# Performance work log

Measured on AMD Instinct MI355X. Metric: run time of the kernel, lower is better.

The kernel has to match this reference:

```python
import jax, jax.numpy as jnp
import numpy as np

N_NODES = 50000
N_EDGES = 800000
D_IN = 64
F1 = 64
F2 = 64
D_HID = 100


def setup_inputs() -> dict:
    key = jax.random.key(0)
    ks = jax.random.split(key, 12)
    x = jax.random.normal(ks[0], (N_NODES, D_IN), dtype=jnp.float32)
    edge_src = jax.random.randint(ks[1], (N_EDGES,), 0, N_NODES, dtype=jnp.int32)
    edge_dst = jax.random.randint(ks[2], (N_EDGES,), 0, N_NODES, dtype=jnp.int32)
    # stands in for pre-normalized GCN adjacency values (D^-1/2 (A+I) D^-1/2)
    edge_weight = jax.random.uniform(ks[3], (N_EDGES,), dtype=jnp.float32)
    def glorot(k, shape):
        lim = np.sqrt(6.0 / (shape[0] + shape[1]))
        return jax.random.uniform(k, shape, jnp.float32, -lim, lim)
    W1 = glorot(ks[4], (D_IN, F1))
    b1 = jnp.zeros((F1,), jnp.float32)
    W2 = glorot(ks[5], (F1, F2))
    b2 = jnp.zeros((F2,), jnp.float32)
    Wd = glorot(ks[6], (F2, D_HID))
    bd = jnp.zeros((D_HID,), jnp.float32)
    Wo = glorot(ks[7], (D_HID, 1))
    bo = jnp.zeros((1,), jnp.float32)
    return {"x": x, "edge_src": edge_src, "edge_dst": edge_dst,
            "edge_weight": edge_weight, "W1": W1, "b1": b1, "W2": W2,
            "b2": b2, "Wd": Wd, "bd": bd, "Wo": Wo, "bo": bo}


def _gcn_conv(x, edge_src, edge_dst, edge_weight, W, b):
    # spektral GCNConv: out = swish(A_norm @ (X @ W) + b)
    h = x @ W                                        # [N, F]
    msg = h[edge_src] * edge_weight[:, None]          # [E, F] gather + scale
    agg = jax.ops.segment_sum(msg, edge_dst, num_segments=N_NODES)  # [N, F]
    return jax.nn.swish(agg + b)


def reference(x, edge_src, edge_dst, edge_weight, W1, b1, W2, b2, Wd, bd, Wo, bo):
    h = _gcn_conv(x, edge_src, edge_dst, edge_weight, W1, b1)
    h = _gcn_conv(h, edge_src, edge_dst, edge_weight, W2, b2)
    h = jax.nn.swish(h @ Wd + bd)                    # Dense(100, swish)
    return jax.nn.sigmoid(h @ Wo + bo)               # Dense(1, sigmoid) -> [N, 1]
```

## Files before the change

### kernel.cpp

```cpp
#include <hip/hip_runtime.h>
#include <hip/hip_fp16.h>

#define N_NODES 50000
#define N_EDGES 800000
#define D 64
#define DHID 100
#define NTILES (N_NODES / 16)
#define NCT 7
#define CAP 32
#define SPILL_MAX 8192
#define NGROUPS 4
#define NSLICES 780
#define FILL_BLOCKS (NGROUPS * NSLICES)
#define MM_BLOCKS ((NTILES + 3) / 4)
#define DST_PER_GROUP (N_NODES / NGROUPS)
#define FSTRIDE (NSLICES * 256)
#define KMAX 5

typedef unsigned short ushort;
typedef unsigned int uint;
typedef __attribute__((ext_vector_type(8))) short s16x8;
typedef __attribute__((ext_vector_type(4))) float f32x4;

#define MFMA16(A, B, C) __builtin_amdgcn_mfma_f32_16x16x32_bf16((A), (B), (C), 0, 0, 0)

__device__ __forceinline__ float swishf(float x) { return x / (1.0f + __expf(-x)); }

__device__ __forceinline__ ushort f2bf(float f) {
    uint u = __float_as_uint(f);
    uint r = (u + 0x7fffu + ((u >> 16) & 1u)) >> 16;
    return (ushort)r;
}
__device__ __forceinline__ float bf2f(ushort h) { return __uint_as_float((uint)h << 16); }
__device__ __forceinline__ float bf_lo(uint d) { return __uint_as_float(d << 16); }
__device__ __forceinline__ float bf_hi(uint d) { return __uint_as_float(d & 0xffff0000u); }

__device__ __forceinline__ float hwf(uint e) {
    return __half2float(__ushort_as_half((ushort)(e >> 16)));
}

__device__ __forceinline__ void accum8(float* acc, uint4 v, float w) {
    acc[0] = fmaf(w, bf_lo(v.x), acc[0]);
    acc[1] = fmaf(w, bf_hi(v.x), acc[1]);
    acc[2] = fmaf(w, bf_lo(v.y), acc[2]);
    acc[3] = fmaf(w, bf_hi(v.y), acc[3]);
    acc[4] = fmaf(w, bf_lo(v.z), acc[4]);
    acc[5] = fmaf(w, bf_hi(v.z), acc[5]);
    acc[6] = fmaf(w, bf_lo(v.w), acc[6]);
    acc[7] = fmaf(w, bf_hi(v.w), acc[7]);
}

__device__ __forceinline__ void gather_body(const ushort* __restrict__ H,
                                            uint4 eA, uint4 eB, int degv,
                                            int j, int fg, float* acc) {
#pragma unroll
    for (int t = 0; t < 8; ++t) acc[t] = 0.f;
    const int sA = j * 4, sB = 16 + j * 4;
    bool pA = sA < degv, pB = sB < degv;
    uint4 vA0, vA1, vA2, vA3, vB0, vB1, vB2, vB3;
    float wA0 = 0, wA1 = 0, wA2 = 0, wA3 = 0;
    float wB0 = 0, wB1 = 0, wB2 = 0, wB3 = 0;
    if (pA) {
        wA0 = hwf(eA.x);
        wA1 = (sA + 1 < degv) ? hwf(eA.y) : 0.f;
        wA2 = (sA + 2 < degv) ? hwf(eA.z) : 0.f;
        wA3 = (sA + 3 < degv) ? hwf(eA.w) : 0.f;
        uint i0 = min(eA.x & 0xffffu, (uint)(N_NODES - 1));
        uint i1 = min(eA.y & 0xffffu, (uint)(N_NODES - 1));
        uint i2 = min(eA.z & 0xffffu, (uint)(N_NODES - 1));
        uint i3 = min(eA.w & 0xffffu, (uint)(N_NODES - 1));
        vA0 = *((const uint4*)(H + ((size_t)i0 << 6) + (fg << 3)));
        vA1 = *((const uint4*)(H + ((size_t)i1 << 6) + (fg << 3)));
        vA2 = *((const uint4*)(H + ((size_t)i2 << 6) + (fg << 3)));
        vA3 = *((const uint4*)(H + ((size_t)i3 << 6) + (fg << 3)));
    }
    if (pB) {
        wB0 = hwf(eB.x);
        wB1 = (sB + 1 < degv) ? hwf(eB.y) : 0.f;
        wB2 = (sB + 2 < degv) ? hwf(eB.z) : 0.f;
        wB3 = (sB + 3 < degv) ? hwf(eB.w) : 0.f;
        uint i0 = min(eB.x & 0xffffu, (uint)(N_NODES - 1));
        uint i1 = min(eB.y & 0xffffu, (uint)(N_NODES - 1));
        uint i2 = min(eB.z & 0xffffu, (uint)(N_NODES - 1));
        uint i3 = min(eB.w & 0xffffu, (uint)(N_NODES - 1));
        vB0 = *((const uint4*)(H + ((size_t)i0 << 6) + (fg << 3)));
        vB1 = *((const uint4*)(H + ((size_t)i1 << 6) + (fg << 3)));
        vB2 = *((const uint4*)(H + ((size_t)i2 << 6) + (fg << 3)));
        vB3 = *((const uint4*)(H + ((size_t)i3 << 6) + (fg << 3)));
    }
    if (pA) {
        accum8(acc, vA0, wA0);
        accum8(acc, vA1, wA1);
        accum8(acc, vA2, wA2);
        accum8(acc, vA3, wA3);
    }
    if (pB) {
        accum8(acc, vB0, wB0);
        accum8(acc, vB1, wB1);
        accum8(acc, vB2, wB2);
        accum8(acc, vB3, wB3);
    }
#pragma unroll
    for (int t = 0; t < 8; ++t) {
        acc[t] += __shfl_xor(acc[t], 8, 64);
        acc[t] += __shfl_xor(acc[t], 16, 64);
    }
}

__device__ __forceinline__ void add_spills(const ushort* __restrict__ H,
                                           const int* __restrict__ spillCnt,
                                           const uint2* __restrict__ spill,
                                           int node, int fg, float* acc) {
    int n = min(*spillCnt, SPILL_MAX);
    for (int i = 0; i < n; ++i) {
        uint2 sp = spill[i];
        if ((int)sp.x == node) {
            float wv = hwf(sp.y);
            uint si = min(sp.y & 0xffffu, (uint)(N_NODES - 1));
            uint4 v = *((const uint4*)(H + ((size_t)si << 6) + (fg << 3)));
            accum8(acc, v, wv);
        }
    }
}

__global__ __launch_bounds__(256) void fill_and_l1(const int* __restrict__ src,
                                                   const int* __restrict__ dst,
                                                   const float* __restrict__ w,
                                                   int* __restrict__ deg,
                                                   uint* __restrict__ csr,
                                                   int* __restrict__ spillCnt,
                                                   uint2* __restrict__ spill,
                                                   const float* __restrict__ X,
                                                   const float* __restrict__ W,
                                                   const float* __restrict__ W2,
                                                   const float* __restrict__ Wd,
                                                   short* __restrict__ W2T2,
                                                   short* __restrict__ WdT2,
                                                   ushort* __restrict__ H) {
    __shared__ __align__(16) short sBT[2][D][72];
    int tid = threadIdx.x;

    if (blockIdx.x < FILL_BLOCKS) {
        const int g = blockIdx.x & (NGROUPS - 1);
        const int s = blockIdx.x >> 2;
        const int lo = g * DST_PER_GROUP;
        const int e0 = s * 256 + tid;
        int d[KMAX];
        bool mk[KMAX];
#pragma unroll
        for (int k = 0; k < KMAX; ++k) {
            int e = e0 + k * FSTRIDE;
            int dv = (e < N_EDGES) ? dst[e] : -1;
            d[k] = dv;
            mk[k] = ((uint)(dv - lo) < (uint)DST_PER_GROUP);
        }
        float wv5[KMAX];
        int sv5[KMAX];
#pragma unroll
        for (int k = 0; k < KMAX; ++k)
            if (mk[k]) {
                int e = e0 + k * FSTRIDE;
                wv5[k] = __builtin_nontemporal_load(w + e);
                sv5[k] = __builtin_nontemporal_load(src + e);
            }
        int r5[KMAX];
#pragma unroll
        for (int k = 0; k < KMAX; ++k)
            if (mk[k]) r5[k] = atomicAdd(&deg[d[k]], 1);
#pragma unroll
        for (int k = 0; k < KMAX; ++k)
            if (mk[k]) {
                uint hw = (uint)__half_as_ushort(__float2half_rn(wv5[k]));
                uint payload = (uint)sv5[k] | (hw << 16);
                int r = r5[k];
                if (r < CAP) {
                    csr[(d[k] << 5) + r] = payload;
                } else {
                    int si = atomicAdd(spillCnt, 1);
                    if (si < SPILL_MAX) spill[si] = make_uint2((uint)d[k], payload);
                }
            }
        return;
    }

    if (blockIdx.x >= FILL_BLOCKS + MM_BLOCKS) {
        if (blockIdx.x == FILL_BLOCKS + MM_BLOCKS) {
            for (int idx = tid; idx < D * D; idx += 256) {
                int k = idx >> 6, c = idx & 63;
                float wv = W2[idx];
                ushort hi = f2bf(wv);
                W2T2[(size_t)c * D + k] = (short)hi;
                W2T2[(size_t)(D + c) * D + k] = (short)f2bf(wv - bf2f(hi));
            }
        } else {
            for (int idx = tid; idx < NCT * 16 * D; idx += 256) {
                int jj = idx >> 6, k = idx & 63;
                float wv = (jj < DHID) ? Wd[k * DHID + jj] : 0.f;
                ushort hi = f2bf(wv);
                WdT2[(size_t)jj * D + k] = (short)hi;
                WdT2[(size_t)(NCT * 16 + jj) * D + k] = (short)f2bf(wv - bf2f(hi));
            }
        }
        return;
    }

    for (int idx = tid; idx < D * D; idx += 256) {
        int k = idx >> 6, c = idx & 63;
        float wv = W[idx];
        ushort hi = f2bf(wv);
        sBT[0][c][k] = (short)hi;
        sBT[1][c][k] = (short)f2bf(wv - bf2f(hi));
    }
    __syncthreads();
    int wv_ = tid >> 6, lane = tid & 63, quad = lane >> 4, m = lane & 15;
    int tile = min((blockIdx.x - FILL_BLOCKS) * 4 + wv_, NTILES - 1);
    int node0 = tile * 16;

    f32x4 acc[4] = {{0,0,0,0},{0,0,0,0},{0,0,0,0},{0,0,0,0}};
#pragma unroll
    for (int kt = 0; kt < 2; ++kt) {
        int k0 = kt * 32 + quad * 8;
        const float* xp = X + ((size_t)(node0 + m) << 6) + k0;
        f32x4 xa = __builtin_nontemporal_load((const f32x4*)xp);
        f32x4 xb = __builtin_nontemporal_load((const f32x4*)(xp + 4));
        float xv[8] = {xa[0], xa[1], xa[2], xa[3], xb[0], xb[1], xb[2], xb[3]};
        s16x8 ahi, alo;
#pragma unroll
        for (int jj = 0; jj < 8; ++jj) {
            ushort hi = f2bf(xv[jj]);
            ahi[jj] = (short)hi;
            alo[jj] = (short)f2bf(xv[jj] - bf2f(hi));
        }
#pragma unroll
        for (int ct = 0; ct < 4; ++ct) {
            int n = ct * 16 + m;
            s16x8 bhi = *((const s16x8*)&sBT[0][n][k0]);
            s16x8 blo = *((const s16x8*)&sBT[1][n][k0]);
            acc[ct] = MFMA16(ahi, bhi, acc[ct]);
            acc[ct] = MFMA16(ahi, blo, acc[ct]);
            acc[ct] = MFMA16(alo, bhi, acc[ct]);
        }
    }
    __syncthreads();
    short (*rep)[16][72] = (short(*)[16][72])&sBT[0][0][0];
#pragma unroll
    for (int ct = 0; ct < 4; ++ct)
#pragma unroll
        for (int r = 0; r < 4; ++r)
            rep[wv_][quad * 4 + r][ct * 16 + m] = (short)f2bf(acc[ct][r]);
#pragma unroll
    for (int half = 0; half < 2; ++half) {
        int r = (lane >> 3) + half * 8;
        int c0 = (lane & 7) * 8;
        s16x8 v = *((const s16x8*)&rep[wv_][r][c0]);
        *((s16x8*)(H + ((size_t)(node0 + r) << 6) + c0)) = v;
    }
}

__global__ __launch_bounds__(256) void gather_act(const ushort* __restrict__ H,
                                                  const int* __restrict__ deg,
                                                  const uint* __restrict__ csr,
                                                  const int* __restrict__ spillCnt,
                                                  const uint2* __restrict__ spill,
                                                  const float* __restrict__ bias,
                                                  ushort* __restrict__ actOut) {
    int tid = threadIdx.x;
    int wave = tid >> 6, lane = tid & 63;
    int h = lane >> 5, j = (lane >> 3) & 3, fg = lane & 7;
    int node = blockIdx.x * 8 + wave * 2 + h;
    const uint* bucket = csr + ((size_t)node << 5);
    uint4 eA = *((const uint4*)(bucket + j * 4));
    uint4 eB = *((const uint4*)(bucket + 16 + j * 4));
    int degv = min(deg[node], CAP);

    float acc[8];
    gather_body(H, eA, eB, degv, j, fg, acc);
    if (j == 0) {
        add_spills(H, spillCnt, spill, node, fg, acc);
        float4 ba = ((const float4*)bias)[fg * 2];
        float4 bb = ((const float4*)bias)[fg * 2 + 1];
        float r0 = swishf(acc[0] + ba.x);
        float r1 = swishf(acc[1] + ba.y);
        float r2 = swishf(acc[2] + ba.z);
        float r3 = swishf(acc[3] + ba.w);
        float r4 = swishf(acc[4] + bb.x);
        float r5 = swishf(acc[5] + bb.y);
        float r6 = swishf(acc[6] + bb.z);
        float r7 = swishf(acc[7] + bb.w);
        uint4 u;
        u.x = (uint)f2bf(r0) | ((uint)f2bf(r1) << 16);
        u.y = (uint)f2bf(r2) | ((uint)f2bf(r3) << 16);
        u.z = (uint)f2bf(r4) | ((uint)f2bf(r5) << 16);
        u.w = (uint)f2bf(r6) | ((uint)f2bf(r7) << 16);
        *((uint4*)(actOut + ((size_t)node << 6) + (fg << 3))) = u;
    }
}

__global__ __launch_bounds__(256) void gather_tail(const ushort* __restrict__ act1,
                                                   const int* __restrict__ deg,
                                                   const uint* __restrict__ csr,
                                                   const int* __restrict__ spillCnt,
                                                   const uint2* __restrict__ spill,
                                                   const short* __restrict__ W2T2,
                                                   const float* __restrict__ b2,
                                                   const short* __restrict__ WdT2,
                                                   const float* __restrict__ bd,
                                                   const float* __restrict__ Wo,
                                                   const float* __restrict__ bo,
                                                   float* __restrict__ out) {
    __shared__ __align__(16) float sAgg[16][72];
    __shared__ __align__(16) short sAct2[16][72];
    __shared__ float sPart[4][16];
    int tid = threadIdx.x;
    int wv = tid >> 6, lane = tid & 63;
    int h = lane >> 5, j = (lane >> 3) & 3, fg = lane & 7;
    int quad = lane >> 4, m = lane & 15;
    int node0 = blockIdx.x * 16;

    {
        int n0l = wv * 4 + h, n1l = wv * 4 + 2 + h;
        int n0 = node0 + n0l, n1 = node0 + n1l;
        const uint* b0 = csr + ((size_t)n0 << 5);
        const uint* b1 = csr + ((size_t)n1 << 5);
        uint4 eA0 = *((const uint4*)(b0 + j * 4));
        uint4 eB0 = *((const uint4*)(b0 + 16 + j * 4));
        uint4 eA1 = *((const uint4*)(b1 + j * 4));
        uint4 eB1 = *((const uint4*)(b1 + 16 + j * 4));
        int d0 = min(deg[n0], CAP);
        int d1 = min(deg[n1], CAP);

        float acc0[8];
        gather_body(act1, eA0, eB0, d0, j, fg, acc0);
        if (j == 0) {
            add_spills(act1, spillCnt, spill, n0, fg, acc0);
            float4 u0 = {acc0[0], acc0[1], acc0[2], acc0[3]};
            float4 u1 = {acc0[4], acc0[5], acc0[6], acc0[7]};
            *((float4*)&sAgg[n0l][fg * 8]) = u0;
            *((float4*)&sAgg[n0l][fg * 8 + 4]) = u1;
        }
        float acc1[8];
        gather_body(act1, eA1, eB1, d1, j, fg, acc1);
        if (j == 0) {
            add_spills(act1, spillCnt, spill, n1, fg, acc1);
            float4 u0 = {acc1[0], acc1[1], acc1[2], acc1[3]};
            float4 u1 = {acc1[4], acc1[5], acc1[6], acc1[7]};
            *((float4*)&sAgg[n1l][fg * 8]) = u0;
            *((float4*)&sAgg[n1l][fg * 8 + 4]) = u1;
        }
    }
    __syncthreads();

    {
        f32x4 acc = {0, 0, 0, 0};
        int n = wv * 16 + m;
#pragma unroll
        for (int kt = 0; kt < 2; ++kt) {
            int k0 = kt * 32 + quad * 8;
            float4 xa = *((const float4*)&sAgg[m][k0]);
            float4 xb = *((const float4*)&sAgg[m][k0 + 4]);
            float xv[8] = {xa.x, xa.y, xa.z, xa.w, xb.x, xb.y, xb.z, xb.w};
            s16x8 ahi, alo;
#pragma unroll
            for (int jj = 0; jj < 8; ++jj) {
                ushort hi = f2bf(xv[jj]);
                ahi[jj] = (short)hi;
                alo[jj] = (short)f2bf(xv[jj] - bf2f(hi));
            }
            s16x8 bhi = *((const s16x8*)(W2T2 + (size_t)n * D + k0));
            s16x8 blo = *((const s16x8*)(W2T2 + (size_t)(D + n) * D + k0));
            acc = MFMA16(ahi, bhi, acc);
            acc = MFMA16(ahi, blo, acc);
            acc = MFMA16(alo, bhi, acc);
        }
        float bv = b2[n];
#pragma unroll
        for (int r = 0; r < 4; ++r)
            sAct2[quad * 4 + r][n] = (short)f2bf(swishf(acc[r] + bv));
    }
    __syncthreads();

    float part[4] = {0, 0, 0, 0};
#pragma unroll
    for (int cc = 0; cc < 2; ++cc) {
        int ct = wv + cc * 4;
        if (ct < NCT) {
            f32x4 acc = {0, 0, 0, 0};
            int n = ct * 16 + m;
#pragma unroll
            for (int kt = 0; kt < 2; ++kt) {
                int k0 = kt * 32 + quad * 8;
                s16x8 a = *((const s16x8*)&sAct2[m][k0]);
                s16x8 bhi = *((const s16x8*)(WdT2 + (size_t)n * D + k0));
                s16x8 blo = *((const s16x8*)(WdT2 + (size_t)(NCT * 16 + n) * D + k0));
                acc = MFMA16(a, bhi, acc);
                acc = MFMA16(a, blo, acc);
            }
            float bdv = (n < DHID) ? bd[n] : 0.f;
            float wov = (n < DHID) ? Wo[n] : 0.f;
#pragma unroll
            for (int r = 0; r < 4; ++r)
                part[r] = fmaf(swishf(acc[r] + bdv), wov, part[r]);
        }
    }
#pragma unroll
    for (int r = 0; r < 4; ++r) {
        part[r] += __shfl_xor(part[r], 1, 64);
        part[r] += __shfl_xor(part[r], 2, 64);
        part[r] += __shfl_xor(part[r], 4, 64);
        part[r] += __shfl_xor(part[r], 8, 64);
    }
    if (m == 0) {
#pragma unroll
        for (int r = 0; r < 4; ++r)
            sPart[wv][quad * 4 + r] = part[r];
    }
    __syncthreads();
    if (tid < 16) {
        float z = sPart[0][tid] + sPart[1][tid] + sPart[2][tid] + sPart[3][tid] + bo[0];
        out[node0 + tid] = 1.f / (1.f + __expf(-z));
    }
}

extern "C" void kernel_launch(void* const* d_in, const int* in_sizes, int n_in,
                              void* d_out, int out_size, void* d_ws, size_t ws_size,
                              hipStream_t stream) {
    const float* x   = (const float*)d_in[0];
    const int* esrc  = (const int*)d_in[1];
    const int* edst  = (const int*)d_in[2];
    const float* ew  = (const float*)d_in[3];
    const float* W1  = (const float*)d_in[4];
    const float* b1  = (const float*)d_in[5];
    const float* W2  = (const float*)d_in[6];
    const float* b2  = (const float*)d_in[7];
    const float* Wd  = (const float*)d_in[8];
    const float* bd  = (const float*)d_in[9];
    const float* Wo  = (const float*)d_in[10];
    const float* bo  = (const float*)d_in[11];
    float* out = (float*)d_out;

    char* ws = (char*)d_ws;
    ushort* H1    = (ushort*)ws; ws += (size_t)N_NODES * D * sizeof(ushort);
    ushort* act1  = (ushort*)ws; ws += (size_t)N_NODES * D * sizeof(ushort);
    uint* csr     = (uint*)ws;   ws += (size_t)N_NODES * CAP * sizeof(uint);
    int* deg      = (int*)ws;    ws += (size_t)N_NODES * sizeof(int);
    int* spillCnt = (int*)ws;    ws += 4 * sizeof(int);
    uint2* spill  = (uint2*)ws;  ws += (size_t)SPILL_MAX * sizeof(uint2);
    short* W2T2   = (short*)ws;  ws += (size_t)2 * D * D * sizeof(short);
    short* WdT2   = (short*)ws;  ws += (size_t)2 * NCT * 16 * D * sizeof(short);

    const int gBlocks = N_NODES / 8;

    hipMemsetAsync(deg, 0, (size_t)(N_NODES + 4) * sizeof(int), stream);

    fill_and_l1<<<FILL_BLOCKS + MM_BLOCKS + 2, 256, 0, stream>>>(
        esrc, edst, ew, deg, csr, spillCnt, spill, x, W1, W2, Wd, W2T2, WdT2, H1);

    gather_act<<<gBlocks, 256, 0, stream>>>(H1, deg, csr, spillCnt, spill, b1, act1);

    gather_tail<<<NTILES, 256, 0, stream>>>(act1, deg, csr, spillCnt, spill,
                                            W2T2, b2, WdT2, bd, Wo, bo, out);
}
```

Baseline: 179.7 us.

## Split feature matrices into 32-wide planes and gather each half separately

Node features are stored as two 32-column bf16 planes so each gather pass touches a 3.2MB working set that fits better in cache, and each layer's aggregation runs as two passes over the halves. The second-layer aggregation is moved out of the MLP head into its own kernels that write fp32 aggregates, followed by a separate mm_head kernel. A block-index swizzle spreads node ranges across XCDs, and results are written with nontemporal stores. In exchange, the CSR buckets are read twice per layer, a 12.8MB fp32 aggregate buffer is written and re-read, and there are more kernel launches.

```diff
diff --git a/kernel.cpp b/kernel.cpp
--- a/kernel.cpp
+++ b/kernel.cpp
@@ -16,11 +16,13 @@
 #define DST_PER_GROUP (N_NODES / NGROUPS)
 #define FSTRIDE (NSLICES * 256)
 #define KMAX 5
+#define GP_BLOCKS 6250
 
 typedef unsigned short ushort;
 typedef unsigned int uint;
 typedef __attribute__((ext_vector_type(8))) short s16x8;
 typedef __attribute__((ext_vector_type(4))) float f32x4;
+typedef __attribute__((ext_vector_type(4))) uint u32x4;
 
 #define MFMA16(A, B, C) __builtin_amdgcn_mfma_f32_16x16x32_bf16((A), (B), (C), 0, 0, 0)
 
@@ -50,74 +52,54 @@
     acc[7] = fmaf(w, bf_hi(v.w), acc[7]);
 }
 
-__device__ __forceinline__ void gather_body(const ushort* __restrict__ H,
-                                            uint4 eA, uint4 eB, int degv,
-                                            int j, int fg, float* acc) {
+__device__ __forceinline__ int swz6250(int bid) {
+    int x = bid & 7, ix = bid >> 3;
+    return x * 781 + (x < 2 ? x : 2) + ix;
+}
+
+__device__ __forceinline__ void gather32(const ushort* __restrict__ plane,
+                                         const uint* __restrict__ bucket,
+                                         int degv, int sj, int fgp, float* acc) {
 #pragma unroll
     for (int t = 0; t < 8; ++t) acc[t] = 0.f;
-    const int sA = j * 4, sB = 16 + j * 4;
-    bool pA = sA < degv, pB = sB < degv;
-    uint4 vA0, vA1, vA2, vA3, vB0, vB1, vB2, vB3;
-    float wA0 = 0, wA1 = 0, wA2 = 0, wA3 = 0;
-    float wB0 = 0, wB1 = 0, wB2 = 0, wB3 = 0;
-    if (pA) {
-        wA0 = hwf(eA.x);
-        wA1 = (sA + 1 < degv) ? hwf(eA.y) : 0.f;
-        wA2 = (sA + 2 < degv) ? hwf(eA.z) : 0.f;
-        wA3 = (sA + 3 < degv) ? hwf(eA.w) : 0.f;
-        uint i0 = min(eA.x & 0xffffu, (uint)(N_NODES - 1));
-        uint i1 = min(eA.y & 0xffffu, (uint)(N_NODES - 1));
-        uint i2 = min(eA.z & 0xffffu, (uint)(N_NODES - 1));
-        uint i3 = min(eA.w & 0xffffu, (uint)(N_NODES - 1));
-        vA0 = *((const uint4*)(H + ((size_t)i0 << 6) + (fg << 3)));
-        vA1 = *((const uint4*)(H + ((size_t)i1 << 6) + (fg << 3)));
-        vA2 = *((const uint4*)(H + ((size_t)i2 << 6) + (fg << 3)));
-        vA3 = *((const uint4*)(H + ((size_t)i3 << 6) + (fg << 3)));
-    }
-    if (pB) {
-        wB0 = hwf(eB.x);
-        wB1 = (sB + 1 < degv) ? hwf(eB.y) : 0.f;
-        wB2 = (sB + 2 < degv) ? hwf(eB.z) : 0.f;
-        wB3 = (sB + 3 < degv) ? hwf(eB.w) : 0.f;
-        uint i0 = min(eB.x & 0xffffu, (uint)(N_NODES - 1));
-        uint i1 = min(eB.y & 0xffffu, (uint)(N_NODES - 1));
-        uint i2 = min(eB.z & 0xffffu, (uint)(N_NODES - 1));
-        uint i3 = min(eB.w & 0xffffu, (uint)(N_NODES - 1));
-        vB0 = *((const uint4*)(H + ((size_t)i0 << 6) + (fg << 3)));
-        vB1 = *((const uint4*)(H + ((size_t)i1 << 6) + (fg << 3)));
-        vB2 = *((const uint4*)(H + ((size_t)i2 << 6) + (fg << 3)));
-        vB3 = *((const uint4*)(H + ((size_t)i3 << 6) + (fg << 3)));
-    }
-    if (pA) {
-        accum8(acc, vA0, wA0);
-        accum8(acc, vA1, wA1);
-        accum8(acc, vA2, wA2);
-        accum8(acc, vA3, wA3);
-    }
-    if (pB) {
-        accum8(acc, vB0, wB0);
-        accum8(acc, vB1, wB1);
-        accum8(acc, vB2, wB2);
-        accum8(acc, vB3, wB3);
+    if (sj < degv) {
+        uint4 e = *((const uint4*)(bucket + sj));
+        float w0 = hwf(e.x);
+        float w1 = (sj + 1 < degv) ? hwf(e.y) : 0.f;
+        float w2 = (sj + 2 < degv) ? hwf(e.z) : 0.f;
+        float w3 = (sj + 3 < degv) ? hwf(e.w) : 0.f;
+        uint i0 = min(e.x & 0xffffu, (uint)(N_NODES - 1));
+        uint i1 = min(e.y & 0xffffu, (uint)(N_NODES - 1));
+        uint i2 = min(e.z & 0xffffu, (uint)(N_NODES - 1));
+        uint i3 = min(e.w & 0xffffu, (uint)(N_NODES - 1));
+        uint4 v0 = *((const uint4*)(plane + ((size_t)i0 << 5) + (fgp << 3)));
+        uint4 v1 = *((const uint4*)(plane + ((size_t)i1 << 5) + (fgp << 3)));
+        uint4 v2 = *((const uint4*)(plane + ((size_t)i2 << 5) + (fgp << 3)));
+        uint4 v3 = *((const uint4*)(plane + ((size_t)i3 << 5) + (fgp << 3)));
+        accum8(acc, v0, w0);
+        accum8(acc, v1, w1);
+        accum8(acc, v2, w2);
+        accum8(acc, v3, w3);
     }
 #pragma unroll
     for (int t = 0; t < 8; ++t) {
+        acc[t] += __shfl_xor(acc[t], 4, 64);
         acc[t] += __shfl_xor(acc[t], 8, 64);
         acc[t] += __shfl_xor(acc[t], 16, 64);
     }
 }
 
-__device__ __forceinline__ void add_spills(const ushort* __restrict__ H,
-                                           const int* __restrict__ spillCnt,
-                                           const uint2* __restrict__ spill,
-                                           int node, int fg, float* acc) {
+__device__ __forceinline__ void add_spills32(const ushort* __restrict__ plane,
+                                             const int* __restrict__ spillCnt,
+                                             const uint2* __restrict__ spill,
+                                             int node, int fgp, float* acc) {
     int n = min(*spillCnt, SPILL_MAX);
     for (int i = 0; i < n; ++i) {
         uint2 sp = spill[i];
         if ((int)sp.x == node) {
             float wv = hwf(sp.y);
             uint si = min(sp.y & 0xffffu, (uint)(N_NODES - 1));
-            uint4 v = *((const uint4*)(H + ((size_t)si << 6) + (fg << 3)));
+            uint4 v = *((const uint4*)(plane + ((size_t)si << 5) + (fgp << 3)));
             accum8(acc, v, wv);
         }
     }
@@ -136,7 +118,8 @@
                                                    const float* __restrict__ Wd,
                                                    short* __restrict__ W2T2,
                                                    short* __restrict__ WdT2,
-                                                   ushort* __restrict__ H) {
+                                                   ushort* __restrict__ H1a,
+                                                   ushort* __restrict__ H1b) {
     __shared__ __align__(16) short sBT[2][D][72];
     int tid = threadIdx.x;
 
@@ -253,32 +236,31 @@
         int r = (lane >> 3) + half * 8;
         int c0 = (lane & 7) * 8;
         s16x8 v = *((const s16x8*)&rep[wv_][r][c0]);
-        *((s16x8*)(H + ((size_t)(node0 + r) << 6) + c0)) = v;
-    }
-}
-
-__global__ __launch_bounds__(256) void gather_act(const ushort* __restrict__ H,
-                                                  const int* __restrict__ deg,
-                                                  const uint* __restrict__ csr,
-                                                  const int* __restrict__ spillCnt,
-                                                  const uint2* __restrict__ spill,
-                                                  const float* __restrict__ bias,
-                                                  ushort* __restrict__ actOut) {
+        ushort* pl = (c0 < 32) ? H1a : H1b;
+        *((s16x8*)(pl + ((size_t)(node0 + r) << 5) + (c0 & 31))) = v;
+    }
+}
+
+__global__ __launch_bounds__(256) void gather_pass_act(const ushort* __restrict__ plane,
+                                                       const int* __restrict__ deg,
+                                                       const uint* __restrict__ csr,
+                                                       const int* __restrict__ spillCnt,
+                                                       const uint2* __restrict__ spill,
+                                                       const float* __restrict__ bias32,
+                                                       ushort* __restrict__ actPlane) {
     int tid = threadIdx.x;
     int wave = tid >> 6, lane = tid & 63;
-    int h = lane >> 5, j = (lane >> 3) & 3, fg = lane & 7;
-    int node = blockIdx.x * 8 + wave * 2 + h;
+    int h = lane >> 5, j = (lane >> 2) & 7, fgp = lane & 3;
+    int node = swz6250(blockIdx.x) * 8 + wave * 2 + h;
     const uint* bucket = csr + ((size_t)node << 5);
-    uint4 eA = *((const uint4*)(bucket + j * 4));
-    uint4 eB = *((const uint4*)(bucket + 16 + j * 4));
     int degv = min(deg[node], CAP);
 
     float acc[8];
-    gather_body(H, eA, eB, degv, j, fg, acc);
+    gather32(plane, bucket, degv, j * 4, fgp, acc);
     if (j == 0) {
-        add_spills(H, spillCnt, spill, node, fg, acc);
-        float4 ba = ((const float4*)bias)[fg * 2];
-        float4 bb = ((const float4*)bias)[fg * 2 + 1];
+        add_spills32(plane, spillCnt, spill, node, fgp, acc);
+        float4 ba = ((const float4*)bias32)[fgp * 2];
+        float4 bb = ((const float4*)bias32)[fgp * 2 + 1];
         float r0 = swishf(acc[0] + ba.x);
         float r1 = swishf(acc[1] + ba.y);
         float r2 = swishf(acc[2] + ba.z);
@@ -287,66 +269,64 @@
         float r5 = swishf(acc[5] + bb.y);
         float r6 = swishf(acc[6] + bb.z);
         float r7 = swishf(acc[7] + bb.w);
-        uint4 u;
-        u.x = (uint)f2bf(r0) | ((uint)f2bf(r1) << 16);
-        u.y = (uint)f2bf(r2) | ((uint)f2bf(r3) << 16);
-        u.z = (uint)f2bf(r4) | ((uint)f2bf(r5) << 16);
-        u.w = (uint)f2bf(r6) | ((uint)f2bf(r7) << 16);
-        *((uint4*)(actOut + ((size_t)node << 6) + (fg << 3))) = u;
-    }
-}
-
-__global__ __launch_bounds__(256) void gather_tail(const ushort* __restrict__ act1,
-                                                   const int* __restrict__ deg,
-                                                   const uint* __restrict__ csr,
-                                                   const int* __restrict__ spillCnt,
-                                                   const uint2* __restrict__ spill,
-                                                   const short* __restrict__ W2T2,
-                                                   const float* __restrict__ b2,
-                                                   const short* __restrict__ WdT2,
-                                                   const float* __restrict__ bd,
-                                                   const float* __restrict__ Wo,
-                                                   const float* __restrict__ bo,
-                                                   float* __restrict__ out) {
+        u32x4 u;
+        u[0] = (uint)f2bf(r0) | ((uint)f2bf(r1) << 16);
+        u[1] = (uint)f2bf(r2) | ((uint)f2bf(r3) << 16);
+        u[2] = (uint)f2bf(r4) | ((uint)f2bf(r5) << 16);
+        u[3] = (uint)f2bf(r6) | ((uint)f2bf(r7) << 16);
+        __builtin_nontemporal_store(u, (u32x4*)(actPlane + ((size_t)node << 5) + (fgp << 3)));
+    }
+}
+
+__global__ __launch_bounds__(256) void gather_pass_agg(const ushort* __restrict__ plane,
+                                                       const int* __restrict__ deg,
+                                                       const uint* __restrict__ csr,
+                                                       const int* __restrict__ spillCnt,
+                                                       const uint2* __restrict__ spill,
+                                                       float* __restrict__ aggPlane) {
+    int tid = threadIdx.x;
+    int wave = tid >> 6, lane = tid & 63;
+    int h = lane >> 5, j = (lane >> 2) & 7, fgp = lane & 3;
+    int node = swz6250(blockIdx.x) * 8 + wave * 2 + h;
+    const uint* bucket = csr + ((size_t)node << 5);
+    int degv = min(deg[node], CAP);
+
+    float acc[8];
+    gather32(plane, bucket, degv, j * 4, fgp, acc);
+    if (j == 0) {
+        add_spills32(plane, spillCnt, spill, node, fgp, acc);
+        f32x4 u0 = {acc[0], acc[1], acc[2], acc[3]};
+        f32x4 u1 = {acc[4], acc[5], acc[6], acc[7]};
+        float* p = aggPlane + ((size_t)node << 5) + (fgp << 3);
+        __builtin_nontemporal_store(u0, (f32x4*)p);
+        __builtin_nontemporal_store(u1, (f32x4*)(p + 4));
+    }
+}
+
+__global__ __launch_bounds__(256) void mm_head(const float* __restrict__ aggA,
+                                               const float* __restrict__ aggB,
+                                               const short* __restrict__ W2T2,
+                                               const float* __restrict__ b2,
+                                               const short* __restrict__ WdT2,
+                                               const float* __restrict__ bd,
+                                               const float* __restrict__ Wo,
+                                               const float* __restrict__ bo,
+                                               float* __restrict__ out) {
     __shared__ __align__(16) float sAgg[16][72];
     __shared__ __align__(16) short sAct2[16][72];
     __shared__ float sPart[4][16];
     int tid = threadIdx.x;
     int wv = tid >> 6, lane = tid & 63;
-    int h = lane >> 5, j = (lane >> 3) & 3, fg = lane & 7;
     int quad = lane >> 4, m = lane & 15;
     int node0 = blockIdx.x * 16;
 
     {
-        int n0l = wv * 4 + h, n1l = wv * 4 + 2 + h;
-        int n0 = node0 + n0l, n1 = node0 + n1l;
-        const uint* b0 = csr + ((size_t)n0 << 5);
-        const uint* b1 = csr + ((size_t)n1 << 5);
-        uint4 eA0 = *((const uint4*)(b0 + j * 4));
-        uint4 eB0 = *((const uint4*)(b0 + 16 + j * 4));
-        uint4 eA1 = *((const uint4*)(b1 + j * 4));
-        uint4 eB1 = *((const uint4*)(b1 + 16 + j * 4));
-        int d0 = min(deg[n0], CAP);
-        int d1 = min(deg[n1], CAP);
-
-        float acc0[8];
-        gather_body(act1, eA0, eB0, d0, j, fg, acc0);
-        if (j == 0) {
-            add_spills(act1, spillCnt, spill, n0, fg, acc0);
-            float4 u0 = {acc0[0], acc0[1], acc0[2], acc0[3]};
-            float4 u1 = {acc0[4], acc0[5], acc0[6], acc0[7]};
-            *((float4*)&sAgg[n0l][fg * 8]) = u0;
-            *((float4*)&sAgg[n0l][fg * 8 + 4]) = u1;
-        }
-        float acc1[8];
-        gather_body(act1, eA1, eB1, d1, j, fg, acc1);
-        if (j == 0) {
-            add_spills(act1, spillCnt, spill, n1, fg, acc1);
-            float4 u0 = {acc1[0], acc1[1], acc1[2], acc1[3]};
-            float4 u1 = {acc1[4], acc1[5], acc1[6], acc1[7]};
-            *((float4*)&sAgg[n1l][fg * 8]) = u0;
-            *((float4*)&sAgg[n1l][fg * 8 + 4]) = u1;
-        }
+        int idx = tid * 4;
+        int nl = idx >> 6, f = idx & 63;
+        const float* p = (f < 32) ? (aggA + ((size_t)(node0 + nl) << 5) + f)
+                                  : (aggB + ((size_t)(node0 + nl) << 5) + (f - 32));
+        float4 v = *((const float4*)p);
+        *((float4*)&sAgg[nl][f]) = v;
     }
     __syncthreads();
 
@@ -439,8 +419,12 @@
     float* out = (float*)d_out;
 
     char* ws = (char*)d_ws;
-    ushort* H1    = (ushort*)ws; ws += (size_t)N_NODES * D * sizeof(ushort);
-    ushort* act1  = (ushort*)ws; ws += (size_t)N_NODES * D * sizeof(ushort);
+    ushort* H1a   = (ushort*)ws; ws += (size_t)N_NODES * 32 * sizeof(ushort);
+    ushort* H1b   = (ushort*)ws; ws += (size_t)N_NODES * 32 * sizeof(ushort);
+    ushort* act1a = (ushort*)ws; ws += (size_t)N_NODES * 32 * sizeof(ushort);
+    ushort* act1b = (ushort*)ws; ws += (size_t)N_NODES * 32 * sizeof(ushort);
+    float* aggA   = (float*)ws;  ws += (size_t)N_NODES * 32 * sizeof(float);
+    float* aggB   = (float*)ws;  ws += (size_t)N_NODES * 32 * sizeof(float);
     uint* csr     = (uint*)ws;   ws += (size_t)N_NODES * CAP * sizeof(uint);
     int* deg      = (int*)ws;    ws += (size_t)N_NODES * sizeof(int);
     int* spillCnt = (int*)ws;    ws += 4 * sizeof(int);
@@ -448,15 +432,16 @@
     short* W2T2   = (short*)ws;  ws += (size_t)2 * D * D * sizeof(short);
     short* WdT2   = (short*)ws;  ws += (size_t)2 * NCT * 16 * D * sizeof(short);
 
-    const int gBlocks = N_NODES / 8;
-
     hipMemsetAsync(deg, 0, (size_t)(N_NODES + 4) * sizeof(int), stream);
 
     fill_and_l1<<<FILL_BLOCKS + MM_BLOCKS + 2, 256, 0, stream>>>(
-        esrc, edst, ew, deg, csr, spillCnt, spill, x, W1, W2, Wd, W2T2, WdT2, H1);
-
-    gather_act<<<gBlocks, 256, 0, stream>>>(H1, deg, csr, spillCnt, spill, b1, act1);
-
-    gather_tail<<<NTILES, 256, 0, stream>>>(act1, deg, csr, spillCnt, spill,
-                                            W2T2, b2, WdT2, bd, Wo, bo, out);
-}
+        esrc, edst, ew, deg, csr, spillCnt, spill, x, W1, W2, Wd, W2T2, WdT2, H1a, H1b);
+
+    gather_pass_act<<<GP_BLOCKS, 256, 0, stream>>>(H1a, deg, csr, spillCnt, spill, b1, act1a);
+    gather_pass_act<<<GP_BLOCKS, 256, 0, stream>>>(H1b, deg, csr, spillCnt, spill, b1 + 32, act1b);
+
+    gather_pass_agg<<<GP_BLOCKS, 256, 0, stream>>>(act1a, deg, csr, spillCnt, spill, aggA);
+    gather_pass_agg<<<GP_BLOCKS, 256, 0, stream>>>(act1b, deg, csr, spillCnt, spill, aggB);
+
+    mm_head<<<NTILES, 256, 0, stream>>>(aggA, aggB, W2T2, b2, WdT2, bd, Wo, bo, out);
+}
```

Result: slower. 209.5 us (+16.6%).
